# Kernel tuning notes

Hardware: AMD Instinct MI355X
Metric: run time of the kernel (lower is better)

The kernel has to match this reference:

```python
import jax, jax.numpy as jnp
import numpy as np

B, V, D, R = 2, 4096, 192, 16
E, H = 2 * D, 8
DH = E // H
K, TK = 16, 8


def _ln(x, g, b):
    m = x.mean(-1, keepdims=True)
    v = ((x - m) ** 2).mean(-1, keepdims=True)
    return (x - m) * jax.lax.rsqrt(v + 1e-5) * g + b


def _coords():
    # voxel centers in [-1,1]^3, (V,3)
    r = (jnp.arange(R, dtype=jnp.float32) + 0.5) / R * 2.0 - 1.0
    return jnp.stack(jnp.meshgrid(r, r, r, indexing='ij'), -1).reshape(-1, 3)


def setup_inputs() -> dict:
    key = jax.random.key(0)
    ks = jax.random.split(key, 10)
    s = 0.02
    return {
        'voxel_tokens': jax.random.normal(ks[0], (B, V, D), jnp.float32),
        'non_empty_mask': jax.random.randint(ks[1], (B, V), 0, 2).astype(bool),
        'We': jax.random.normal(ks[2], (D, E)) * s, 'be': jnp.zeros((E,)),
        'g1': jnp.ones((E,)), 'bt1': jnp.zeros((E,)),
        'Wqkv': jax.random.normal(ks[3], (E, 3 * E)) * s, 'bqkv': jnp.zeros((3 * E,)),
        'Wo': jax.random.normal(ks[4], (E, E)) * s, 'bo': jnp.zeros((E,)),
        'Wc': jax.random.normal(ks[5], (E, D)) * s, 'bc': jnp.zeros((D,)),
        'g2': jnp.ones((E,)), 'bt2': jnp.zeros((E,)),
        'W1': jax.random.normal(ks[6], (E, 2 * E)) * s, 'b1': jnp.zeros((2 * E,)),
        'W2': jax.random.normal(ks[7], (2 * E, E)) * s, 'b2': jnp.zeros((E,)),
    }


def reference(voxel_tokens, non_empty_mask, We, be, g1, bt1, Wqkv, bqkv, Wo, bo,
              Wc, bc, g2, bt2, W1, b1, W2, b2):
    fmask = non_empty_mask.astype(voxel_tokens.dtype)  # (B,V)
    shortcut = voxel_tokens
    x = voxel_tokens @ We + be                          # expand: (B,V,E)
    x = _ln(x, g1, bt1)
    # --- sparse dynamic voxel attention ---
    c = _coords()
    d2 = jnp.sum((c[:, None, :] - c[None, :, :]) ** 2, -1)  # (V,V)
    big = jnp.asarray(1e9, x.dtype)
    dmask = d2[None] + (1.0 - fmask)[:, None, :] * big      # empty keys pushed away
    _, knn = jax.lax.top_k(-dmask, K)                        # (B,V,K) nearest non-empty
    qkv = x @ Wqkv + bqkv
    q, k, v = jnp.split(qkv, 3, axis=-1)                     # (B,V,E) each
    bidx = jnp.arange(B)[:, None, None]
    kn = k[bidx, knn].reshape(B, V, K, H, DH)                # gathered neighbor keys
    vn = v[bidx, knn].reshape(B, V, K, H, DH)
    qh = q.reshape(B, V, H, DH)
    scores = jnp.einsum('bvhd,bvkhd->bvhk', qh, kn) / jnp.sqrt(jnp.asarray(DH, x.dtype))
    nvalid = fmask[bidx, knn]                                # (B,V,K)
    scores = jnp.where(nvalid[:, :, None, :] > 0, scores, -big)
    sel, sidx = jax.lax.top_k(scores, TK)                    # top_k_select by score
    attn = jax.nn.softmax(sel, axis=-1)                      # (B,V,H,TK)
    vt = vn.transpose(0, 1, 3, 2, 4)                         # (B,V,H,K,DH)
    vsel = jnp.take_along_axis(vt, sidx[..., None], axis=3)  # (B,V,H,TK,DH)
    o = jnp.einsum('bvhk,bvhkd->bvhd', attn, vsel).reshape(B, V, E)
    o = o @ Wo + bo
    # masked scatter: empty voxels -> zeros (reconstruct_dense_masked_scatter_2)
    x = o * fmask[..., None]
    x = x @ Wc + bc                                          # contract
    x = x * 0.5 + shortcut                                   # DropPath(0) -> identity
    x2 = x @ We + be
    x2 = _ln(x2, g2, bt2)
    x2 = jax.nn.gelu(x2 @ W1 + b1) @ W2 + b2                 # FeedForward(E, 2E)
    x2 = x2 @ Wc + bc
    return x2 * 0.5 + x
```

## Files before the change

### kernel.cpp

```cpp
#include <hip/hip_runtime.h>
#include <stdint.h>


using u16 = unsigned short;
using u32 = unsigned int;
using u64 = unsigned long long;

typedef short short8 __attribute__((ext_vector_type(8)));
typedef float f32x4 __attribute__((ext_vector_type(4)));

#define DEV static __device__ __forceinline__

constexpr int cV = 4096, cD = 192;
constexpr int cE = 384;
constexpr int cKN = 16, cTK = 8;
constexpr int cM = 2 * cV;
constexpr int c3E = 1152;

DEV float bf2f(u16 v) { return __uint_as_float(((u32)v) << 16); }
DEV float bflo(u32 v) { return __uint_as_float(v << 16); }
DEV float bfhi(u32 v) { return __uint_as_float(v & 0xFFFF0000u); }
DEV u16 f2bf(float f) {
  u32 u = __float_as_uint(f);
  u = (u + 0x7FFFu + ((u >> 16) & 1u)) >> 16;
  return (u16)u;
}
DEV int mget(const void* mp, int flag, int i) {
  if (flag == 0) return ((const int*)mp)[i] != 0;
  if (flag == 1) return ((const float*)mp)[i] != 0.0f;
  if (flag == 2) return ((const u16*)mp)[i] != 0;
  return ((const unsigned char*)mp)[i] != 0;
}
DEV float gelu_tanh(float x) {
  float t = tanhf(0.7978845608028654f * (x + 0.044715f * x * x * x));
  return 0.5f * x * (1.0f + t);
}
DEV u32 f2ord(float f) {
  u32 u = __float_as_uint(f);
  return (u & 0x80000000u) ? ~u : (u | 0x80000000u);
}
DEV float ord2f(u32 o) {
  u32 bits = (o & 0x80000000u) ? (o & 0x7FFFFFFFu) : ~o;
  return __uint_as_float(bits);
}
DEV int bf_plausible(u32 h) {
  if (h == 0u || h == 0x8000u) return 1;
  u32 e = (h >> 7) & 0xFFu;
  return (e >= 100u && e <= 140u) ? 1 : 0;
}

using as1p = const unsigned int __attribute__((address_space(1)))*;
using as3p = unsigned int __attribute__((address_space(3)))*;
DEV void gload16(const void* g, void* l) {
  __builtin_amdgcn_global_load_lds((as1p)g, (as3p)l, 16, 0, 0);
}
DEV f32x4 mfma16x16x32_bf16(short8 a, short8 b, f32x4 c) {
  asm volatile("v_mfma_f32_16x16x32_bf16 %0, %1, %2, %0" : "+v"(c) : "v"(a), "v"(b));
  return c;
}
DEV int swz(int row, int byteoff) { return byteoff ^ ((row & 7) << 4); }
DEV int ldswz(int r, int c) { return r * 64 + (c ^ ((r & 7) * 8)); }

#define SBPIN() __builtin_amdgcn_sched_barrier(0)
#define VMW(N) do { \
  __builtin_amdgcn_sched_barrier(0); \
  asm volatile("s_waitcnt vmcnt(" #N ")" ::: "memory"); \
  __builtin_amdgcn_sched_barrier(0); \
} while (0)

template <int T, typename AF>
DEV void stage_1x8(const u16* __restrict__ wbase, int Kst, u16* bpriv,
                   int l15, int l4, int sr, int scs,
                   f32x4 (&acc)[2][3], AF&& aread) {
  #pragma unroll
  for (int i = 0; i < 6; ++i)
    gload16(wbase + (size_t)(i * 8 + sr) * Kst + scs, (char*)bpriv + i * 1024);
  SBPIN();
  #pragma unroll
  for (int t = 0; t < T; ++t) {
    if (t + 1 < T) {
      #pragma unroll
      for (int i = 0; i < 6; ++i)
        gload16(wbase + (size_t)(i * 8 + sr) * Kst + (t + 1) * 64 + scs,
                (char*)bpriv + ((t + 1) & 1) * 6144 + i * 1024);
      VMW(6);
    } else {
      VMW(0);
    }
    const u16* bb = bpriv + (t & 1) * 3072;
    #pragma unroll
    for (int ks = 0; ks < 2; ++ks) {
      short8 a0 = aread(0, t, ks);
      short8 a1 = aread(1, t, ks);
      #pragma unroll
      for (int n = 0; n < 3; ++n) {
        short8 b = *(const short8*)&bb[ldswz(n * 16 + l15, ks * 32 + l4 * 8)];
        acc[0][n] = mfma16x16x32_bf16(a0, b, acc[0][n]);
        acc[1][n] = mfma16x16x32_bf16(a1, b, acc[1][n]);
      }
    }
    SBPIN();
  }
}

template <int T, typename AF>
DEV void stage_2x4(const u16* __restrict__ wbase, int Kst, u16* bpriv,
                   int l15, int l4, int sr, int scs,
                   f32x4 (&acc)[3], AF&& aread) {
  #pragma unroll
  for (int i = 0; i < 6; ++i)
    gload16(wbase + (size_t)(i * 8 + sr) * Kst + scs, (char*)bpriv + i * 1024);
  SBPIN();
  #pragma unroll
  for (int t = 0; t < T; ++t) {
    if (t + 1 < T) {
      #pragma unroll
      for (int i = 0; i < 6; ++i)
        gload16(wbase + (size_t)(i * 8 + sr) * Kst + (t + 1) * 64 + scs,
                (char*)bpriv + ((t + 1) & 1) * 6144 + i * 1024);
      VMW(6);
    } else {
      VMW(0);
    }
    const u16* bb = bpriv + (t & 1) * 3072;
    #pragma unroll
    for (int ks = 0; ks < 2; ++ks) {
      short8 a = aread(t, ks);
      #pragma unroll
      for (int n = 0; n < 3; ++n) {
        short8 b = *(const short8*)&bb[ldswz(n * 16 + l15, ks * 32 + l4 * 8)];
        acc[n] = mfma16x16x32_bf16(a, b, acc[n]);
      }
    }
    SBPIN();
  }
}

__global__ void detect_all_kernel(const u32* __restrict__ tok,
                                  const u32* __restrict__ m,
                                  int* __restrict__ flag) {
  __shared__ int cnt, sa, sb, sc;
  if (threadIdx.x == 0) { cnt = 0; sa = 0; sb = 0; sc = 0; }
  __syncthreads();
  int c = 0;
  for (int i = threadIdx.x; i < 4096; i += 256) {
    u32 d = tok[i];
    c += bf_plausible(d & 0xFFFFu) & bf_plausible(d >> 16);
  }
  atomicAdd(&cnt, c);
  int a = 0, b = 0, cc = 0;
  for (int i = threadIdx.x; i < 2048; i += 256) {
    u32 d = m[i];
    if (!(d == 0u || d == 1u)) a = 1;
    if (!(d == 0u || d == 0x3F800000u)) b = 1;
    if (!(d == 0u || d == 0x00003F80u || d == 0x3F800000u || d == 0x3F803F80u)) cc = 1;
  }
  if (a) atomicOr(&sa, 1);
  if (b) atomicOr(&sb, 1);
  if (cc) atomicOr(&sc, 1);
  __syncthreads();
  if (threadIdx.x == 0) {
    flag[1] = (cnt > 3400) ? 1 : 0;
    flag[0] = (sa == 0) ? 0 : ((sb == 0) ? 1 : ((sc == 0) ? 2 : 3));
  }
}

struct PrepArgs {
  const void* csrc[11]; u16* cdst[11]; int cn[11];
  const void* tsrc[6]; u16* tdst[6]; int tK[6]; int tN[6];
  const void* mask; u64* bm;
};
__global__ __launch_bounds__(256) void prep_kernel(PrepArgs a, const int* __restrict__ flag) {
  const int job = blockIdx.y;
  const int dt = flag[1];
  if (job < 11) {
    const int n = a.cn[job];
    u16* d = a.cdst[job];
    if (dt) {
      const u16* s = (const u16*)a.csrc[job];
      for (int i = blockIdx.x * 256 + threadIdx.x; i < n; i += gridDim.x * 256) d[i] = s[i];
    } else {
      const float* s = (const float*)a.csrc[job];
      for (int i = blockIdx.x * 256 + threadIdx.x; i < n; i += gridDim.x * 256) d[i] = f2bf(s[i]);
    }
  } else if (job < 17) {
    const int t = job - 11;
    const int K = a.tK[t], N = a.tN[t];
    const int total = K * N;
    u16* d = a.tdst[t];
    for (int i = blockIdx.x * 256 + threadIdx.x; i < total; i += gridDim.x * 256) {
      int n = i / K, k = i - n * K;
      u16 vv;
      if (dt) vv = ((const u16*)a.tsrc[t])[(size_t)k * N + n];
      else vv = f2bf(((const float*)a.tsrc[t])[(size_t)k * N + n]);
      d[i] = vv;
    }
  } else {
    const int gw = (blockIdx.x * 256 + threadIdx.x) >> 6;
    const int lane = threadIdx.x & 63;
    if (gw < 128) {
      const int fl = flag[0];
      u64 bal = __ballot(mget(a.mask, fl, gw * 64 + lane) != 0);
      if (lane == 0) a.bm[gw] = bal;
    }
  }
}

__global__ __launch_bounds__(256) void knn_kernel(const u64* __restrict__ bitmask,
                                                  int* __restrict__ knn_out) {
  const int tid = threadIdx.x;
  const int wid = tid >> 6, lane = tid & 63;
  const int q0 = blockIdx.x * 4;
  const int b = q0 >> 12;
  const int q = q0 + wid;
  const int v = q & 4095;
  __shared__ u64 smask[64];
  __shared__ int hist4[4][64];
  __shared__ int listT[4][64];
  __shared__ int out16s[4][16];
  __shared__ int meta[4][3];
  __shared__ int cntA[4], cntT[4];
  if (tid < 64) smask[tid] = bitmask[b * 64 + tid];
  for (int i = tid; i < 4 * 64; i += 256) ((int*)hist4)[i] = 0;
  if (lane == 0) { cntA[wid] = 0; cntT[wid] = 0; }
  __syncthreads();
  const int iv = v >> 8, jv = (v >> 4) & 15, kv = v & 15;
  #pragma unroll
  for (int t = 0; t < 12; ++t) {
    int o = t * 64 + lane;
    if (o < 729) {
      int oi = o / 81, rm = o - oi * 81;
      int oj = rm / 9, ok = rm - oj * 9;
      int i = iv + oi - 4, j = jv + oj - 4, k = kv + ok - 4;
      if (((i | j | k) & ~15) == 0) {
        int u = (i << 8) | (j << 4) | k;
        if ((smask[u >> 6] >> (u & 63)) & 1ull) {
          int di = oi - 4, dj = oj - 4, dk = ok - 4;
          atomicAdd(&hist4[wid][di * di + dj * dj + dk * dk], 1);
        }
      }
    }
  }
  __syncthreads();
  if (lane == 0) {
    int cum = 0, T = -1, below = 0;
    for (int d = 0; d <= 48; ++d) {
      int h = hist4[wid][d];
      if (h > 0 && cum + h >= cKN) { T = d; below = cum; break; }
      cum += h;
    }
    if (T > 24) T = -1;
    meta[wid][0] = T; meta[wid][1] = below; meta[wid][2] = (T < 0) ? 1 : 0;
  }
  __syncthreads();
  const int T = meta[wid][0], below = meta[wid][1], fb = meta[wid][2];
  #pragma unroll
  for (int t = 0; t < 12; ++t) {
    int o = t * 64 + lane;
    if (o < 729) {
      int oi = o / 81, rm = o - oi * 81;
      int oj = rm / 9, ok = rm - oj * 9;
      int i = iv + oi - 4, j = jv + oj - 4, k = kv + ok - 4;
      if (((i | j | k) & ~15) == 0) {
        int u = (i << 8) | (j << 4) | k;
        if ((smask[u >> 6] >> (u & 63)) & 1ull) {
          int di = oi - 4, dj = oj - 4, dk = ok - 4;
          int d2 = di * di + dj * dj + dk * dk;
          if (d2 < T) { int p = atomicAdd(&cntA[wid], 1); out16s[wid][p] = u; }
          else if (d2 == T) { int p = atomicAdd(&cntT[wid], 1); if (p < 64) listT[wid][p] = u; }
        }
      }
    }
  }
  __syncthreads();
  if (!fb) {
    if (lane == 0) {
      int need = cKN - below;
      int nT = cntT[wid] < 64 ? cntT[wid] : 64;
      for (int r = 0; r < need; ++r) {
        int bi = 0, bu = 0x7FFFFFFF;
        for (int i2 = 0; i2 < nT; ++i2) { int x = listT[wid][i2]; if (x < bu) { bu = x; bi = i2; } }
        out16s[wid][below + r] = bu;
        listT[wid][bi] = 0x7FFFFFFF;
      }
    }
  } else {
    u64 rem = smask[lane];
    const int myi = lane >> 2;
    const int di2 = (iv - myi) * (iv - myi);
    for (int r = 0; r < cKN; ++r) {
      u64 tmp = rem;
      u32 best = 0xFFFFFFFFu;
      while (tmp) {
        int bp = __builtin_ctzll(tmp);
        tmp &= tmp - 1;
        int u = (lane << 6) | bp;
        int dj = jv - ((u >> 4) & 15), dk = kv - (u & 15);
        u32 key = (u32)(((di2 + dj * dj + dk * dk) << 12) | u);
        if (key < best) best = key;
      }
      u32 pk = (best == 0xFFFFFFFFu) ? 0xFFFFFFFFu : ((best << 6) | (u32)lane);
      #pragma unroll
      for (int off = 1; off < 64; off <<= 1) {
        u32 o2 = __shfl_xor(pk, off);
        if (o2 < pk) pk = o2;
      }
      int u = (int)((pk >> 6) & 4095u);
      int wl = (int)(pk & 63u);
      if (lane == wl) rem &= ~(1ull << (u & 63));
      if (lane == 0) out16s[wid][r] = u;
    }
  }
  __syncthreads();
  if (lane < cKN) knn_out[q * cKN + lane] = out16s[wid][lane];
}

__global__ __launch_bounds__(512) void fused_ln_qkv(
    const u16* __restrict__ tokc, const u16* __restrict__ WeT,
    const u16* __restrict__ be, const u16* __restrict__ g1, const u16* __restrict__ bt1,
    const u16* __restrict__ WqkvT, const u16* __restrict__ bqkv,
    u16* __restrict__ QB) {
  __shared__ alignas(16) u16 Afull[3 * 2048];
  __shared__ alignas(16) u16 Bst[8][2][3072];
  __shared__ alignas(16) char X1[32 * 768];
  __shared__ float st[32][8][2];
  const int tid = threadIdx.x;
  const int lane = tid & 63, wn = tid >> 6;
  const int l15 = lane & 15, l4 = lane >> 4;
  const int sr = lane >> 3;
  const int scs = (((lane & 7) ^ sr) << 3);
  const int row0 = blockIdx.x * 32;
  u16* bpriv = &Bst[wn][0][0];

  for (int g = wn; g < 12; g += 8)
    gload16(tokc + (size_t)(row0 + (g & 3) * 8 + sr) * 192 + (g >> 2) * 64 + scs,
            (char*)Afull + g * 1024);
  SBPIN();
  __syncthreads();

  f32x4 acc[2][3];
  #pragma unroll
  for (int m = 0; m < 2; ++m)
    #pragma unroll
    for (int n = 0; n < 3; ++n) acc[m][n] = f32x4{0.f, 0.f, 0.f, 0.f};
  stage_1x8<3>(WeT + (size_t)(wn * 48) * 192, 192, bpriv, l15, l4, sr, scs, acc,
               [&](int m, int t, int ks) {
                 return *(const short8*)&Afull[t * 2048 + ldswz(m * 16 + l15, ks * 32 + l4 * 8)];
               });
  float s[2][4], sq[2][4];
  #pragma unroll
  for (int m = 0; m < 2; ++m)
    #pragma unroll
    for (int j = 0; j < 4; ++j) { s[m][j] = 0.f; sq[m][j] = 0.f; }
  #pragma unroll
  for (int n = 0; n < 3; ++n) {
    const float bi = bf2f(be[wn * 48 + n * 16 + l15]);
    #pragma unroll
    for (int m = 0; m < 2; ++m)
      #pragma unroll
      for (int j = 0; j < 4; ++j) {
        acc[m][n][j] += bi;
        s[m][j] += acc[m][n][j]; sq[m][j] += acc[m][n][j] * acc[m][n][j];
      }
  }
  #pragma unroll
  for (int off = 1; off < 16; off <<= 1)
    #pragma unroll
    for (int m = 0; m < 2; ++m)
      #pragma unroll
      for (int j = 0; j < 4; ++j) { s[m][j] += __shfl_xor(s[m][j], off); sq[m][j] += __shfl_xor(sq[m][j], off); }
  if (l15 == 0) {
    #pragma unroll
    for (int m = 0; m < 2; ++m)
      #pragma unroll
      for (int j = 0; j < 4; ++j) {
        const int rl = m * 16 + l4 * 4 + j;
        st[rl][wn][0] = s[m][j]; st[rl][wn][1] = sq[m][j];
      }
  }
  __syncthreads();
  #pragma unroll
  for (int m = 0; m < 2; ++m)
    #pragma unroll
    for (int j = 0; j < 4; ++j) {
      const int rl = m * 16 + l4 * 4 + j;
      float ts = 0.f, tq = 0.f;
      #pragma unroll
      for (int wv = 0; wv < 8; ++wv) { ts += st[rl][wv][0]; tq += st[rl][wv][1]; }
      const float mean = ts * (1.0f / 384.0f);
      const float var = tq * (1.0f / 384.0f) - mean * mean;
      const float rstd = rsqrtf(var + 1e-5f);
      #pragma unroll
      for (int n = 0; n < 3; ++n) {
        const int col = wn * 48 + n * 16 + l15;
        const float v = (acc[m][n][j] - mean) * rstd * bf2f(g1[col]) + bf2f(bt1[col]);
        *(u16*)(X1 + swz(rl, rl * 768 + col * 2)) = f2bf(v);
      }
    }
  __syncthreads();

  for (int chunk = 0; chunk < 3; ++chunk) {
    f32x4 a2[2][3];
    #pragma unroll
    for (int m = 0; m < 2; ++m)
      #pragma unroll
      for (int n = 0; n < 3; ++n) a2[m][n] = f32x4{0.f, 0.f, 0.f, 0.f};
    stage_1x8<6>(WqkvT + (size_t)(chunk * 384 + wn * 48) * 384, 384, bpriv,
                 l15, l4, sr, scs, a2,
                 [&](int m, int t, int ks) {
                   const int rl = m * 16 + l15;
                   return *(const short8*)(X1 + swz(rl, rl * 768 + (t * 64 + ks * 32 + l4 * 8) * 2));
                 });
    #pragma unroll
    for (int n = 0; n < 3; ++n) {
      const int col = chunk * 384 + wn * 48 + n * 16 + l15;
      const float bi = bf2f(bqkv[col]);
      #pragma unroll
      for (int m = 0; m < 2; ++m)
        #pragma unroll
        for (int j = 0; j < 4; ++j)
          QB[(size_t)(row0 + m * 16 + l4 * 4 + j) * c3E + col] = f2bf(a2[m][n][j] + bi);
    }
  }
}

__global__ __launch_bounds__(512) void fused_mid(
    const u16* __restrict__ S2, const u16* __restrict__ WoT, const u16* __restrict__ bo,
    const void* __restrict__ mask, const int* __restrict__ flag,
    const u16* __restrict__ WcT, const u16* __restrict__ bc, const u16* __restrict__ tokc,
    float* __restrict__ XM,
    const u16* __restrict__ WeT, const u16* __restrict__ be,
    const u16* __restrict__ g2, const u16* __restrict__ bt2, u16* __restrict__ S1out) {
  __shared__ alignas(16) u16 Afull[6 * 2048];
  __shared__ alignas(16) u16 Bst[8][2][3072];
  __shared__ alignas(16) char Tb[32 * 768];
  __shared__ float st[32][8][2];
  char* X2 = Tb;
  const int tid = threadIdx.x;
  const int lane = tid & 63, wn = tid >> 6;
  const int wr = wn >> 2, wc = wn & 3;
  const int l15 = lane & 15, l4 = lane >> 4;
  const int sr = lane >> 3;
  const int scs = (((lane & 7) ^ sr) << 3);
  const int row0 = blockIdx.x * 32;
  const int fl = flag[0];
  u16* bpriv = &Bst[wn][0][0];

  for (int g = wn; g < 24; g += 8)
    gload16(S2 + (size_t)(row0 + (g & 3) * 8 + sr) * cE + (g >> 2) * 64 + scs,
            (char*)Afull + g * 1024);
  SBPIN();
  __syncthreads();

  {
    f32x4 acc[2][3];
    #pragma unroll
    for (int m = 0; m < 2; ++m)
      #pragma unroll
      for (int n = 0; n < 3; ++n) acc[m][n] = f32x4{0.f, 0.f, 0.f, 0.f};
    stage_1x8<6>(WoT + (size_t)(wn * 48) * 384, 384, bpriv, l15, l4, sr, scs, acc,
                 [&](int m, int t, int ks) {
                   return *(const short8*)&Afull[t * 2048 + ldswz(m * 16 + l15, ks * 32 + l4 * 8)];
                 });
    #pragma unroll
    for (int m = 0; m < 2; ++m)
      #pragma unroll
      for (int j = 0; j < 4; ++j) {
        const int rl = m * 16 + l4 * 4 + j;
        const float fm = mget(mask, fl, row0 + rl) ? 1.0f : 0.0f;
        #pragma unroll
        for (int n = 0; n < 3; ++n) {
          const int col = wn * 48 + n * 16 + l15;
          const float v = (acc[m][n][j] + bf2f(bo[col])) * fm;
          *(u16*)(Tb + swz(rl, rl * 768 + col * 2)) = f2bf(v);
        }
      }
  }
  __syncthreads();

  f32x4 a2[3];
  #pragma unroll
  for (int n = 0; n < 3; ++n) a2[n] = f32x4{0.f, 0.f, 0.f, 0.f};
  stage_2x4<6>(WcT + (size_t)(wc * 48) * 384, 384, bpriv, l15, l4, sr, scs, a2,
               [&](int t, int ks) {
                 const int rl = wr * 16 + l15;
                 return *(const short8*)(Tb + swz(rl, rl * 768 + (t * 64 + ks * 32 + l4 * 8) * 2));
               });
  __syncthreads();
  #pragma unroll
  for (int n = 0; n < 3; ++n) {
    const int col = wc * 48 + n * 16 + l15;
    const float bi = bf2f(bc[col]);
    #pragma unroll
    for (int j = 0; j < 4; ++j) {
      const int rl = wr * 16 + l4 * 4 + j;
      const size_t oi = (size_t)(row0 + rl) * cD + col;
      const float r = (a2[n][j] + bi) * 0.5f + bf2f(tokc[oi]);
      XM[oi] = r;
      *(u16*)(X2 + swz(rl, rl * 384 + col * 2)) = f2bf(r);
    }
  }
  __syncthreads();

  {
    f32x4 a3[2][3];
    #pragma unroll
    for (int m = 0; m < 2; ++m)
      #pragma unroll
      for (int n = 0; n < 3; ++n) a3[m][n] = f32x4{0.f, 0.f, 0.f, 0.f};
    stage_1x8<3>(WeT + (size_t)(wn * 48) * 192, 192, bpriv, l15, l4, sr, scs, a3,
                 [&](int m, int t, int ks) {
                   const int rl = m * 16 + l15;
                   return *(const short8*)(X2 + swz(rl, rl * 384 + (t * 64 + ks * 32 + l4 * 8) * 2));
                 });
    float s[2][4], sq[2][4];
    #pragma unroll
    for (int m = 0; m < 2; ++m)
      #pragma unroll
      for (int j = 0; j < 4; ++j) { s[m][j] = 0.f; sq[m][j] = 0.f; }
    #pragma unroll
    for (int n = 0; n < 3; ++n) {
      const float bi = bf2f(be[wn * 48 + n * 16 + l15]);
      #pragma unroll
      for (int m = 0; m < 2; ++m)
        #pragma unroll
        for (int j = 0; j < 4; ++j) {
          a3[m][n][j] += bi;
          s[m][j] += a3[m][n][j]; sq[m][j] += a3[m][n][j] * a3[m][n][j];
        }
    }
    #pragma unroll
    for (int off = 1; off < 16; off <<= 1)
      #pragma unroll
      for (int m = 0; m < 2; ++m)
        #pragma unroll
        for (int j = 0; j < 4; ++j) { s[m][j] += __shfl_xor(s[m][j], off); sq[m][j] += __shfl_xor(sq[m][j], off); }
    if (l15 == 0) {
      #pragma unroll
      for (int m = 0; m < 2; ++m)
        #pragma unroll
        for (int j = 0; j < 4; ++j) {
          const int rl = m * 16 + l4 * 4 + j;
          st[rl][wn][0] = s[m][j]; st[rl][wn][1] = sq[m][j];
        }
    }
    __syncthreads();
    #pragma unroll
    for (int m = 0; m < 2; ++m)
      #pragma unroll
      for (int j = 0; j < 4; ++j) {
        const int rl = m * 16 + l4 * 4 + j;
        float ts = 0.f, tq = 0.f;
        #pragma unroll
        for (int wv = 0; wv < 8; ++wv) { ts += st[rl][wv][0]; tq += st[rl][wv][1]; }
        const float mean = ts * (1.0f / 384.0f);
        const float var = tq * (1.0f / 384.0f) - mean * mean;
        const float rstd = rsqrtf(var + 1e-5f);
        #pragma unroll
        for (int n = 0; n < 3; ++n) {
          const int col = wn * 48 + n * 16 + l15;
          S1out[(size_t)(row0 + rl) * cE + col] =
              f2bf((a3[m][n][j] - mean) * rstd * bf2f(g2[col]) + bf2f(bt2[col]));
        }
      }
  }
}

__global__ __launch_bounds__(512) void fused_ffn(
    const u16* __restrict__ S1, const u16* __restrict__ W1T, const u16* __restrict__ b1,
    const u16* __restrict__ W2T, const u16* __restrict__ b2,
    const u16* __restrict__ WcT, const u16* __restrict__ bc,
    const float* __restrict__ XM, void* __restrict__ outv, const int* __restrict__ flag) {
  __shared__ alignas(16) u16 Afull[6 * 2048];
  __shared__ alignas(16) u16 Bst[8][2][3072];
  __shared__ alignas(16) char Hb[32 * 768];
  const int tid = threadIdx.x;
  const int lane = tid & 63, wn = tid >> 6;
  const int wr = wn >> 2, wc = wn & 3;
  const int l15 = lane & 15, l4 = lane >> 4;
  const int sr = lane >> 3;
  const int scs = (((lane & 7) ^ sr) << 3);
  const int row0 = blockIdx.x * 32;
  u16* bpriv = &Bst[wn][0][0];

  for (int g = wn; g < 24; g += 8)
    gload16(S1 + (size_t)(row0 + (g & 3) * 8 + sr) * cE + (g >> 2) * 64 + scs,
            (char*)Afull + g * 1024);
  SBPIN();
  __syncthreads();

  f32x4 accF[2][3];
  #pragma unroll
  for (int m = 0; m < 2; ++m)
    #pragma unroll
    for (int n = 0; n < 3; ++n) accF[m][n] = f32x4{0.f, 0.f, 0.f, 0.f};

  for (int half = 0; half < 2; ++half) {
    {
      f32x4 a1[2][3];
      #pragma unroll
      for (int m = 0; m < 2; ++m)
        #pragma unroll
        for (int n = 0; n < 3; ++n) a1[m][n] = f32x4{0.f, 0.f, 0.f, 0.f};
      stage_1x8<6>(W1T + (size_t)(half * 384 + wn * 48) * 384, 384, bpriv,
                   l15, l4, sr, scs, a1,
                   [&](int m, int t, int ks) {
                     return *(const short8*)&Afull[t * 2048 + ldswz(m * 16 + l15, ks * 32 + l4 * 8)];
                   });
      #pragma unroll
      for (int n = 0; n < 3; ++n) {
        const int col = wn * 48 + n * 16 + l15;
        const float bi = bf2f(b1[half * 384 + col]);
        #pragma unroll
        for (int m = 0; m < 2; ++m)
          #pragma unroll
          for (int j = 0; j < 4; ++j) {
            const int rl = m * 16 + l4 * 4 + j;
            *(u16*)(Hb + swz(rl, rl * 768 + col * 2)) = f2bf(gelu_tanh(a1[m][n][j] + bi));
          }
      }
    }
    __syncthreads();
    stage_1x8<6>(W2T + (size_t)(wn * 48) * 768 + half * 384, 768, bpriv,
                 l15, l4, sr, scs, accF,
                 [&](int m, int t, int ks) {
                   const int rl = m * 16 + l15;
                   return *(const short8*)(Hb + swz(rl, rl * 768 + (t * 64 + ks * 32 + l4 * 8) * 2));
                 });
    __syncthreads();
  }
  #pragma unroll
  for (int n = 0; n < 3; ++n) {
    const int col = wn * 48 + n * 16 + l15;
    const float bi = bf2f(b2[col]);
    #pragma unroll
    for (int m = 0; m < 2; ++m)
      #pragma unroll
      for (int j = 0; j < 4; ++j) {
        const int rl = m * 16 + l4 * 4 + j;
        *(u16*)(Hb + swz(rl, rl * 768 + col * 2)) = f2bf(accF[m][n][j] + bi);
      }
  }
  __syncthreads();
  f32x4 a3[3];
  #pragma unroll
  for (int n = 0; n < 3; ++n) a3[n] = f32x4{0.f, 0.f, 0.f, 0.f};
  stage_2x4<6>(WcT + (size_t)(wc * 48) * 384, 384, bpriv, l15, l4, sr, scs, a3,
               [&](int t, int ks) {
                 const int rl = wr * 16 + l15;
                 return *(const short8*)(Hb + swz(rl, rl * 768 + (t * 64 + ks * 32 + l4 * 8) * 2));
               });
  u16* o16 = (u16*)outv;
  float* o32 = (float*)outv;
  const int dtf = flag[1];
  #pragma unroll
  for (int n = 0; n < 3; ++n) {
    const int col = wc * 48 + n * 16 + l15;
    const float bi = bf2f(bc[col]);
    #pragma unroll
    for (int j = 0; j < 4; ++j) {
      const int rl = wr * 16 + l4 * 4 + j;
      const size_t oi = (size_t)(row0 + rl) * cD + col;
      const float r = (a3[n][j] + bi) * 0.5f + XM[oi];
      if (dtf) o16[oi] = f2bf(r);
      else o32[oi] = r;
    }
  }
}

__global__ __launch_bounds__(256) void attn_kernel(const u16* __restrict__ qkv,
                                                   const int* __restrict__ knn,
                                                   u16* __restrict__ o_out) {
  const int wid = threadIdx.x >> 6;
  const int lane = threadIdx.x & 63;
  const int bq = blockIdx.x * 4 + wid;
  const int b = bq >> 12;
  __shared__ float w4[4][8][8];
  __shared__ int vid4[4][8][8];
  __shared__ int nb4[4][16];
  float (*w)[8] = w4[wid];
  int (*vid)[8] = vid4[wid];
  int* nb = nb4[wid];
  if (lane < 16) nb[lane] = knn[bq * cKN + lane];
  const int h = lane >> 3;
  const int j = lane & 7;
  const uint2* qp = (const uint2*)(qkv + (size_t)bq * c3E + h * 48);
  const int r0 = nb[j], r1 = nb[j + 8];
  const uint2* k0p = (const uint2*)(qkv + ((size_t)(b * cV + r0)) * c3E + cE + h * 48);
  const uint2* k1p = (const uint2*)(qkv + ((size_t)(b * cV + r1)) * c3E + cE + h * 48);
  float s0 = 0.f, s1 = 0.f;
  #pragma unroll
  for (int t = 0; t < 12; ++t) {
    uint2 qv = qp[t];
    uint2 k0 = k0p[t];
    uint2 k1 = k1p[t];
    s0 += bflo(qv.x) * bflo(k0.x) + bfhi(qv.x) * bfhi(k0.x)
        + bflo(qv.y) * bflo(k0.y) + bfhi(qv.y) * bfhi(k0.y);
    s1 += bflo(qv.x) * bflo(k1.x) + bfhi(qv.x) * bfhi(k1.x)
        + bflo(qv.y) * bflo(k1.y) + bfhi(qv.y) * bfhi(k1.y);
  }
  const float inv = 0.14433756729740643f;
  u64 key0 = (((u64)f2ord(s0 * inv)) << 4) | (u64)(15 - j);
  u64 key1 = (((u64)f2ord(s1 * inv)) << 4) | (u64)(15 - (j + 8));
  float m0 = 0.f, Z = 0.f, myw = 0.f;
  int myv = 0;
  #pragma unroll
  for (int r = 0; r < cTK; ++r) {
    u64 best = key0 > key1 ? key0 : key1;
    u64 o1 = __shfl_xor(best, 1); if (o1 > best) best = o1;
    u64 o2 = __shfl_xor(best, 2); if (o2 > best) best = o2;
    u64 o4 = __shfl_xor(best, 4); if (o4 > best) best = o4;
    if (key0 == best) key0 = 0;
    if (key1 == best) key1 = 0;
    float sv = ord2f((u32)(best >> 4));
    int nsel = 15 - (int)(best & 15ull);
    if (r == 0) m0 = sv;
    float e = expf(sv - m0);
    Z += e;
    if (j == r) { myw = e; myv = nsel; }
  }
  w[h][j] = myw / Z;
  vid[h][j] = nb[myv];
  const u16* vbase = qkv + (size_t)(b * cV) * c3E + 2 * cE;
  #pragma unroll
  for (int rep = 0; rep < 6; ++rep) {
    int e = rep * 64 + lane;
    int h2 = e / 48;
    float acc = 0.f;
    #pragma unroll
    for (int t = 0; t < cTK; ++t)
      acc += w[h2][t] * bf2f(vbase[(size_t)vid[h2][t] * c3E + e]);
    o_out[(size_t)bq * cE + e] = f2bf(acc);
  }
}

extern "C" void kernel_launch(void* const* d_in, const int* in_sizes, int n_in,
                              void* d_out, int out_size, void* d_ws, size_t ws_size,
                              hipStream_t stream) {
  if (n_in < 18) return;
  const void* mask = d_in[1];

  char* ws = (char*)d_ws;
  size_t off = 0;
  auto alloc = [&](size_t bytes) { size_t o = off; off += (bytes + 255) & ~(size_t)255; return o; };
  int* flag  = (int*)(ws + alloc(256));
  u64* bmask = (u64*)(ws + alloc(128 * 8));
  int* knn   = (int*)(ws + alloc((size_t)cM * cKN * 4));
  float* XM  = (float*)(ws + alloc((size_t)cM * cD * 4));
  u16* S1    = (u16*)(ws + alloc((size_t)cM * cE * 2));
  u16* S2    = (u16*)(ws + alloc((size_t)cM * cE * 2));
  u16* QB    = (u16*)(ws + alloc((size_t)cM * c3E * 2));
  u16* tokc  = (u16*)(ws + alloc((size_t)cM * cD * 2));
  u16* be    = (u16*)(ws + alloc(cE * 2));
  u16* g1    = (u16*)(ws + alloc(cE * 2));
  u16* bt1   = (u16*)(ws + alloc(cE * 2));
  u16* bqkv  = (u16*)(ws + alloc(c3E * 2));
  u16* bo    = (u16*)(ws + alloc(cE * 2));
  u16* bc    = (u16*)(ws + alloc(cD * 2));
  u16* g2    = (u16*)(ws + alloc(cE * 2));
  u16* bt2   = (u16*)(ws + alloc(cE * 2));
  u16* b1    = (u16*)(ws + alloc(2 * cE * 2));
  u16* b2    = (u16*)(ws + alloc(cE * 2));
  u16* WeT   = (u16*)(ws + alloc((size_t)384 * 192 * 2));
  u16* WqkvT = (u16*)(ws + alloc((size_t)1152 * 384 * 2));
  u16* WoT   = (u16*)(ws + alloc((size_t)384 * 384 * 2));
  u16* WcT   = (u16*)(ws + alloc((size_t)256 * 384 * 2));
  u16* W1T   = (u16*)(ws + alloc((size_t)768 * 384 * 2));
  u16* W2T   = (u16*)(ws + alloc((size_t)384 * 768 * 2));
  (void)ws_size; (void)in_sizes; (void)out_size;

  detect_all_kernel<<<1, 256, 0, stream>>>((const u32*)d_in[0], (const u32*)mask, flag);

  {
    PrepArgs pa;
    const int csrci[11] = {0, 3, 4, 5, 7, 9, 11, 12, 13, 15, 17};
    u16* cdsts[11] = {tokc, be, g1, bt1, bqkv, bo, bc, g2, bt2, b1, b2};
    const int cns[11] = {cM * cD, cE, cE, cE, c3E, cE, cD, cE, cE, 2 * cE, cE};
    for (int i = 0; i < 11; ++i) { pa.csrc[i] = d_in[csrci[i]]; pa.cdst[i] = cdsts[i]; pa.cn[i] = cns[i]; }
    const int tsrci[6] = {2, 6, 8, 10, 14, 16};
    u16* tdsts[6] = {WeT, WqkvT, WoT, WcT, W1T, W2T};
    const int tKs[6] = {192, 384, 384, 384, 384, 768};
    const int tNs[6] = {384, 1152, 384, 192, 768, 384};
    for (int i = 0; i < 6; ++i) { pa.tsrc[i] = d_in[tsrci[i]]; pa.tdst[i] = tdsts[i]; pa.tK[i] = tKs[i]; pa.tN[i] = tNs[i]; }
    pa.mask = mask; pa.bm = bmask;
    prep_kernel<<<dim3(96, 18), 256, 0, stream>>>(pa, flag);
  }

  knn_kernel<<<cM / 4, 256, 0, stream>>>(bmask, knn);

  const int GB = cM / 32;
  fused_ln_qkv<<<GB, 512, 0, stream>>>(tokc, WeT, be, g1, bt1, WqkvT, bqkv, QB);
  attn_kernel<<<cM / 4, 256, 0, stream>>>(QB, knn, S2);
  fused_mid<<<GB, 512, 0, stream>>>(S2, WoT, bo, mask, flag, WcT, bc, tokc, XM,
                                    WeT, be, g2, bt2, S1);
  fused_ffn<<<GB, 512, 0, stream>>>(S1, W1T, b1, W2T, b2, WcT, bc, XM, d_out, flag);
}
```

Before: 155.0 us.

## Fuse mid and FFN kernels, keep residual and LN output on chip

Merges the post-attention kernel and the FFN kernel into one launch. The LN2 output now stays in shared memory instead of going through the global S1 buffer, and the residual stays in registers instead of the fp32 XM buffer. This removes one launch and the global write and read of both intermediates. In exchange, the fused kernel uses more registers for the held residual, and the shared buffers are reused (the hidden buffer aliases Afull), which adds synchronisation-ordering risk.

```diff
diff --git a/kernel.cpp b/kernel.cpp
--- a/kernel.cpp
+++ b/kernel.cpp
@@ -424,18 +424,20 @@
   }
 }
 
-__global__ __launch_bounds__(512) void fused_mid(
+__global__ __launch_bounds__(512) void fused_cd(
     const u16* __restrict__ S2, const u16* __restrict__ WoT, const u16* __restrict__ bo,
     const void* __restrict__ mask, const int* __restrict__ flag,
     const u16* __restrict__ WcT, const u16* __restrict__ bc, const u16* __restrict__ tokc,
-    float* __restrict__ XM,
     const u16* __restrict__ WeT, const u16* __restrict__ be,
-    const u16* __restrict__ g2, const u16* __restrict__ bt2, u16* __restrict__ S1out) {
+    const u16* __restrict__ g2, const u16* __restrict__ bt2,
+    const u16* __restrict__ W1T, const u16* __restrict__ b1,
+    const u16* __restrict__ W2T, const u16* __restrict__ b2,
+    void* __restrict__ outv) {
   __shared__ alignas(16) u16 Afull[6 * 2048];
   __shared__ alignas(16) u16 Bst[8][2][3072];
   __shared__ alignas(16) char Tb[32 * 768];
   __shared__ float st[32][8][2];
-  char* X2 = Tb;
+  char* HbA = (char*)Afull;
   const int tid = threadIdx.x;
   const int lane = tid & 63, wn = tid >> 6;
   const int wr = wn >> 2, wc = wn & 3;
@@ -478,10 +480,10 @@
   }
   __syncthreads();
 
-  f32x4 a2[3];
-  #pragma unroll
-  for (int n = 0; n < 3; ++n) a2[n] = f32x4{0.f, 0.f, 0.f, 0.f};
-  stage_2x4<6>(WcT + (size_t)(wc * 48) * 384, 384, bpriv, l15, l4, sr, scs, a2,
+  f32x4 xm[3];
+  #pragma unroll
+  for (int n = 0; n < 3; ++n) xm[n] = f32x4{0.f, 0.f, 0.f, 0.f};
+  stage_2x4<6>(WcT + (size_t)(wc * 48) * 384, 384, bpriv, l15, l4, sr, scs, xm,
                [&](int t, int ks) {
                  const int rl = wr * 16 + l15;
                  return *(const short8*)(Tb + swz(rl, rl * 768 + (t * 64 + ks * 32 + l4 * 8) * 2));
@@ -494,10 +496,8 @@
     #pragma unroll
     for (int j = 0; j < 4; ++j) {
       const int rl = wr * 16 + l4 * 4 + j;
-      const size_t oi = (size_t)(row0 + rl) * cD + col;
-      const float r = (a2[n][j] + bi) * 0.5f + bf2f(tokc[oi]);
-      XM[oi] = r;
-      *(u16*)(X2 + swz(rl, rl * 384 + col * 2)) = f2bf(r);
+      xm[n][j] = (xm[n][j] + bi) * 0.5f + bf2f(tokc[(size_t)(row0 + rl) * cD + col]);
+      *(u16*)(Tb + swz(rl, rl * 384 + col * 2)) = f2bf(xm[n][j]);
     }
   }
   __syncthreads();
@@ -511,7 +511,7 @@
     stage_1x8<3>(WeT + (size_t)(wn * 48) * 192, 192, bpriv, l15, l4, sr, scs, a3,
                  [&](int m, int t, int ks) {
                    const int rl = m * 16 + l15;
-                   return *(const short8*)(X2 + swz(rl, rl * 384 + (t * 64 + ks * 32 + l4 * 8) * 2));
+                   return *(const short8*)(Tb + swz(rl, rl * 384 + (t * 64 + ks * 32 + l4 * 8) * 2));
                  });
     float s[2][4], sq[2][4];
     #pragma unroll
@@ -559,34 +559,11 @@
         #pragma unroll
         for (int n = 0; n < 3; ++n) {
           const int col = wn * 48 + n * 16 + l15;
-          S1out[(size_t)(row0 + rl) * cE + col] =
-              f2bf((a3[m][n][j] - mean) * rstd * bf2f(g2[col]) + bf2f(bt2[col]));
+          const float v = (a3[m][n][j] - mean) * rstd * bf2f(g2[col]) + bf2f(bt2[col]);
+          *(u16*)(Tb + swz(rl, rl * 768 + col * 2)) = f2bf(v);
         }
       }
   }
-}
-
-__global__ __launch_bounds__(512) void fused_ffn(
-    const u16* __restrict__ S1, const u16* __restrict__ W1T, const u16* __restrict__ b1,
-    const u16* __restrict__ W2T, const u16* __restrict__ b2,
-    const u16* __restrict__ WcT, const u16* __restrict__ bc,
-    const float* __restrict__ XM, void* __restrict__ outv, const int* __restrict__ flag) {
-  __shared__ alignas(16) u16 Afull[6 * 2048];
-  __shared__ alignas(16) u16 Bst[8][2][3072];
-  __shared__ alignas(16) char Hb[32 * 768];
-  const int tid = threadIdx.x;
-  const int lane = tid & 63, wn = tid >> 6;
-  const int wr = wn >> 2, wc = wn & 3;
-  const int l15 = lane & 15, l4 = lane >> 4;
-  const int sr = lane >> 3;
-  const int scs = (((lane & 7) ^ sr) << 3);
-  const int row0 = blockIdx.x * 32;
-  u16* bpriv = &Bst[wn][0][0];
-
-  for (int g = wn; g < 24; g += 8)
-    gload16(S1 + (size_t)(row0 + (g & 3) * 8 + sr) * cE + (g >> 2) * 64 + scs,
-            (char*)Afull + g * 1024);
-  SBPIN();
   __syncthreads();
 
   f32x4 accF[2][3];
@@ -605,7 +582,8 @@
       stage_1x8<6>(W1T + (size_t)(half * 384 + wn * 48) * 384, 384, bpriv,
                    l15, l4, sr, scs, a1,
                    [&](int m, int t, int ks) {
-                     return *(const short8*)&Afull[t * 2048 + ldswz(m * 16 + l15, ks * 32 + l4 * 8)];
+                     const int rl = m * 16 + l15;
+                     return *(const short8*)(Tb + swz(rl, rl * 768 + (t * 64 + ks * 32 + l4 * 8) * 2));
                    });
       #pragma unroll
       for (int n = 0; n < 3; ++n) {
@@ -616,7 +594,7 @@
           #pragma unroll
           for (int j = 0; j < 4; ++j) {
             const int rl = m * 16 + l4 * 4 + j;
-            *(u16*)(Hb + swz(rl, rl * 768 + col * 2)) = f2bf(gelu_tanh(a1[m][n][j] + bi));
+            *(u16*)(HbA + swz(rl, rl * 768 + col * 2)) = f2bf(gelu_tanh(a1[m][n][j] + bi));
           }
       }
     }
@@ -625,7 +603,7 @@
                  l15, l4, sr, scs, accF,
                  [&](int m, int t, int ks) {
                    const int rl = m * 16 + l15;
-                   return *(const short8*)(Hb + swz(rl, rl * 768 + (t * 64 + ks * 32 + l4 * 8) * 2));
+                   return *(const short8*)(HbA + swz(rl, rl * 768 + (t * 64 + ks * 32 + l4 * 8) * 2));
                  });
     __syncthreads();
   }
@@ -638,7 +616,7 @@
       #pragma unroll
       for (int j = 0; j < 4; ++j) {
         const int rl = m * 16 + l4 * 4 + j;
-        *(u16*)(Hb + swz(rl, rl * 768 + col * 2)) = f2bf(accF[m][n][j] + bi);
+        *(u16*)(HbA + swz(rl, rl * 768 + col * 2)) = f2bf(accF[m][n][j] + bi);
       }
   }
   __syncthreads();
@@ -648,7 +626,7 @@
   stage_2x4<6>(WcT + (size_t)(wc * 48) * 384, 384, bpriv, l15, l4, sr, scs, a3,
                [&](int t, int ks) {
                  const int rl = wr * 16 + l15;
-                 return *(const short8*)(Hb + swz(rl, rl * 768 + (t * 64 + ks * 32 + l4 * 8) * 2));
+                 return *(const short8*)(HbA + swz(rl, rl * 768 + (t * 64 + ks * 32 + l4 * 8) * 2));
                });
   u16* o16 = (u16*)outv;
   float* o32 = (float*)outv;
@@ -661,7 +639,7 @@
     for (int j = 0; j < 4; ++j) {
       const int rl = wr * 16 + l4 * 4 + j;
       const size_t oi = (size_t)(row0 + rl) * cD + col;
-      const float r = (a3[n][j] + bi) * 0.5f + XM[oi];
+      const float r = (a3[n][j] + bi) * 0.5f + xm[n][j];
       if (dtf) o16[oi] = f2bf(r);
       else o32[oi] = r;
     }
@@ -746,8 +724,6 @@
   int* flag  = (int*)(ws + alloc(256));
   u64* bmask = (u64*)(ws + alloc(128 * 8));
   int* knn   = (int*)(ws + alloc((size_t)cM * cKN * 4));
-  float* XM  = (float*)(ws + alloc((size_t)cM * cD * 4));
-  u16* S1    = (u16*)(ws + alloc((size_t)cM * cE * 2));
   u16* S2    = (u16*)(ws + alloc((size_t)cM * cE * 2));
   u16* QB    = (u16*)(ws + alloc((size_t)cM * c3E * 2));
   u16* tokc  = (u16*)(ws + alloc((size_t)cM * cD * 2));
@@ -791,7 +767,6 @@
   const int GB = cM / 32;
   fused_ln_qkv<<<GB, 512, 0, stream>>>(tokc, WeT, be, g1, bt1, WqkvT, bqkv, QB);
   attn_kernel<<<cM / 4, 256, 0, stream>>>(QB, knn, S2);
-  fused_mid<<<GB, 512, 0, stream>>>(S2, WoT, bo, mask, flag, WcT, bc, tokc, XM,
-                                    WeT, be, g2, bt2, S1);
-  fused_ffn<<<GB, 512, 0, stream>>>(S1, W1T, b1, W2T, b2, WcT, bc, XM, d_out, flag);
-}
+  fused_cd<<<GB, 512, 0, stream>>>(S2, WoT, bo, mask, flag, WcT, bc, tokc,
+                                   WeT, be, g2, bt2, W1T, b1, W2T, b2, d_out);
+}
```

Measured after the change: 150.9 us. 2.6% less time.
